# Optimization experiments

Measured on AMD Instinct MI355X. Metric: run time of the kernel, lower is better.

## Reference

```python
import jax, jax.numpy as jnp
import numpy as np

DIM = 1024
NHEAD = 16
HEAD_DIM = DIM // NHEAD
B, S, L = 1, 4096, 4096


def setup_inputs() -> dict:
    key = jax.random.key(0)
    ks = jax.random.split(key, 11)
    scale = 1.0 / np.sqrt(DIM)
    inp = {
        'query': jax.random.normal(ks[0], (B, S, DIM), dtype=jnp.float32),
        'key': jax.random.normal(ks[1], (B, L, DIM), dtype=jnp.float32),
        'value': jax.random.normal(ks[2], (B, L, DIM), dtype=jnp.float32),
        # torch nn.Linear weights: y = x @ W.T + b, W shape (out, in) = (DIM, DIM)
        'Wq': jax.random.normal(ks[3], (DIM, DIM), dtype=jnp.float32) * scale,
        'bq': jax.random.normal(ks[4], (DIM,), dtype=jnp.float32) * 0.01,
        'Wk': jax.random.normal(ks[5], (DIM, DIM), dtype=jnp.float32) * scale,
        'bk': jax.random.normal(ks[6], (DIM,), dtype=jnp.float32) * 0.01,
        'Wv': jax.random.normal(ks[7], (DIM, DIM), dtype=jnp.float32) * scale,
        'bv': jax.random.normal(ks[8], (DIM,), dtype=jnp.float32) * 0.01,
        'Wo': jax.random.normal(ks[9], (DIM, DIM), dtype=jnp.float32) * scale,
        'bo': jax.random.normal(ks[10], (DIM,), dtype=jnp.float32) * 0.01,
    }
    return inp


def _split_heads(x):
    # (B, T, D) -> (B, H, T, hd)
    b, t, _ = x.shape
    return x.reshape(b, t, NHEAD, HEAD_DIM).transpose(0, 2, 1, 3)


def reference(query, key, value, Wq, bq, Wk, bk, Wv, bv, Wo, bo):
    q = _split_heads(query @ Wq.T + bq)   # (B,H,S,hd)
    k = _split_heads(key @ Wk.T + bk)     # (B,H,L,hd)
    v = _split_heads(value @ Wv.T + bv)   # (B,H,L,hd)
    inv_sqrt_d = 1.0 / np.sqrt(HEAD_DIM).astype(np.float32)
    scores = jnp.einsum('bhsd,bhld->bhsl', q, k) * inv_sqrt_d
    probs = jax.nn.softmax(scores, axis=-1)
    ctx = jnp.einsum('bhsl,bhld->bhsd', probs, v)
    ctx = ctx.transpose(0, 2, 1, 3).reshape(query.shape[0], -1, DIM)
    return ctx @ Wo.T + bo
```

## Files before the change

kernel.cpp:

```cpp
#include <hip/hip_runtime.h>
#include <hip/hip_bf16.h>

#define DIM 1024
#define NHEAD 16
#define HD 64
#define SEQ 4096

typedef unsigned short u16;
typedef unsigned int u32;
typedef __attribute__((ext_vector_type(8))) short bf16x8;
typedef __attribute__((ext_vector_type(4))) float f32x4;
typedef __attribute__((ext_vector_type(16))) float f32x16;

__device__ __forceinline__ u16 f2bf(float x) {
  __hip_bfloat16 h = __float2bfloat16(x);
  return *reinterpret_cast<u16*>(&h);
}

__device__ __forceinline__ float bf2f(u16 u) {
  union { u32 u; float f; } c;
  c.u = ((u32)u) << 16;
  return c.f;
}

__device__ __forceinline__ float fexp2(float x) {
#if __has_builtin(__builtin_amdgcn_exp2f)
  return __builtin_amdgcn_exp2f(x);
#else
  return __expf(x * 0.69314718056f);
#endif
}

__device__ __forceinline__ u32 cvtpk(float a, float b) {
  u32 r;
  asm("v_cvt_pk_bf16_f32 %0, %1, %2" : "=v"(r) : "v"(a), "v"(b));
  return r;
}

__device__ __forceinline__ void pswap(u32& a, u32& b) {
  asm("v_permlane32_swap_b32 %0, %1" : "+v"(a), "+v"(b));
}

__device__ __forceinline__ void gload16(const u16* g, const u16* l) {
  __builtin_amdgcn_global_load_lds(
      (const __attribute__((address_space(1))) void*)g,
      (__attribute__((address_space(3))) void*)l, 16, 0, 0);
}

__device__ __forceinline__ float vsum16(const f32x16& v) {
  float a[8];
#pragma unroll
  for (int j = 0; j < 8; ++j) a[j] = v[j] + v[j + 8];
#pragma unroll
  for (int j = 0; j < 4; ++j) a[j] = a[j] + a[j + 4];
  return (a[0] + a[2]) + (a[1] + a[3]);
}

__global__ __launch_bounds__(256) void cvt_all(
    const float* __restrict__ q, const float* __restrict__ k, const float* __restrict__ v,
    const float* __restrict__ wq, const float* __restrict__ wk, const float* __restrict__ wv,
    const float* __restrict__ wo,
    u16* __restrict__ oq, u16* __restrict__ ok, u16* __restrict__ ov,
    u16* __restrict__ owq, u16* __restrict__ owk, u16* __restrict__ owv, u16* __restrict__ owo) {
  int b = blockIdx.x;
  const float* in;
  u16* out;
  int i;
  if (b < 12288) {
    int s = b >> 12;
    in = (s == 0) ? q : (s == 1) ? k : v;
    out = (s == 0) ? oq : (s == 1) ? ok : ov;
    i = (b & 4095) * 256 + threadIdx.x;
  } else {
    int bb = b - 12288;
    int s = bb >> 10;
    in = (s == 0) ? wq : (s == 1) ? wk : (s == 2) ? wv : wo;
    out = (s == 0) ? owq : (s == 1) ? owk : (s == 2) ? owv : owo;
    i = (bb & 1023) * 256 + threadIdx.x;
  }
  float4 val = ((const float4*)in)[i];
  ushort4 o;
  o.x = f2bf(val.x); o.y = f2bf(val.y); o.z = f2bf(val.z); o.w = f2bf(val.w);
  ((ushort4*)out)[i] = o;
}

__global__ __launch_bounds__(256, 3) void gemm_proj(
    const u16* __restrict__ qx, const u16* __restrict__ kx, const u16* __restrict__ vx,
    const u16* __restrict__ wqp, const u16* __restrict__ wkp, const u16* __restrict__ wvp,
    const float* __restrict__ bq, const float* __restrict__ bk, const float* __restrict__ bv,
    u16* __restrict__ Qb, u16* __restrict__ Kb, u16* __restrict__ Vt) {
  __shared__ u16 As[128][64];
  __shared__ u16 Bs[128][64];
  const int z = blockIdx.y;
  const u16 *Ag, *Bg;
  const float* bias;
  u16* outp;
  int mb, nb;
  float scale = 1.f;
  if (z == 0) {
    Ag = qx; Bg = wqp; bias = bq; outp = Qb;
    mb = blockIdx.x >> 3; nb = blockIdx.x & 7; scale = 0.18033688f;
  } else if (z == 1) {
    Ag = kx; Bg = wkp; bias = bk; outp = Kb;
    mb = blockIdx.x >> 3; nb = blockIdx.x & 7;
  } else {
    Ag = wvp; Bg = vx; bias = bv; outp = Vt;
    mb = blockIdx.x >> 5; nb = blockIdx.x & 31;
  }

  const int tid = threadIdx.x, lane = tid & 63, wid = tid >> 6;
  const int lq = lane & 15, g = lane >> 4;
  const int wr = wid >> 1, wc = wid & 1;
  const int m0 = mb * 128, n0 = nb * 128;
  const int sr = lane >> 3, ss = lane & 7;

  const u16* pA = Ag + (size_t)(m0 + wid * 32 + sr) * DIM + ((ss ^ sr) * 8);
  const u16* pB = Bg + (size_t)(n0 + wid * 32 + sr) * DIM + ((ss ^ sr) * 8);

  const f32x4 zero4 = {0.f, 0.f, 0.f, 0.f};
  f32x4 acc[4][4];
#pragma unroll
  for (int mi = 0; mi < 4; ++mi)
#pragma unroll
    for (int ni = 0; ni < 4; ++ni) acc[mi][ni] = zero4;

  for (int k0 = 0; k0 < DIM; k0 += 64) {
    __syncthreads();
#pragma unroll
    for (int i = 0; i < 4; ++i) {
      gload16(pA + i * 8 * DIM + k0, &As[wid * 32 + i * 8][0]);
      gload16(pB + i * 8 * DIM + k0, &Bs[wid * 32 + i * 8][0]);
    }
    __syncthreads();
#pragma unroll
    for (int kk = 0; kk < 2; ++kk) {
      bf16x8 a[4], b[4];
#pragma unroll
      for (int t4 = 0; t4 < 4; ++t4) {
        u32 offA = (u32)(wr * 64 + t4 * 16 + lq) * 128 + (u32)(((kk * 4 + g) ^ (lq & 7)) * 16);
        u32 offB = (u32)(wc * 64 + t4 * 16 + lq) * 128 + (u32)(((kk * 4 + g) ^ (lq & 7)) * 16);
        a[t4] = *(const bf16x8*)((const char*)As + offA);
        b[t4] = *(const bf16x8*)((const char*)Bs + offB);
      }
#pragma unroll
      for (int mi = 0; mi < 4; ++mi)
#pragma unroll
        for (int ni = 0; ni < 4; ++ni)
          acc[mi][ni] = __builtin_amdgcn_mfma_f32_16x16x32_bf16(a[mi], b[ni], acc[mi][ni], 0, 0, 0);
    }
  }

  if (z < 2) {
    float bn[4];
#pragma unroll
    for (int ni = 0; ni < 4; ++ni) bn[ni] = bias[n0 + wc * 64 + ni * 16 + lq];
#pragma unroll
    for (int mi = 0; mi < 4; ++mi)
#pragma unroll
      for (int r = 0; r < 4; ++r) {
        int mm = m0 + wr * 64 + mi * 16 + g * 4 + r;
#pragma unroll
        for (int ni = 0; ni < 4; ++ni) {
          int nn = n0 + wc * 64 + ni * 16 + lq;
          float v = (acc[mi][ni][r] + bn[ni]) * scale;
          outp[((size_t)(nn >> 6) * SEQ + mm) * 64 + (nn & 63)] = f2bf(v);
        }
      }
  } else {
#pragma unroll
    for (int mi = 0; mi < 4; ++mi)
#pragma unroll
      for (int r = 0; r < 4; ++r) {
        int mm = m0 + wr * 64 + mi * 16 + g * 4 + r;
        float bm = bias[mm];
#pragma unroll
        for (int ni = 0; ni < 4; ++ni) {
          int nn = n0 + wc * 64 + ni * 16 + lq;
          outp[(size_t)mm * SEQ + nn] = f2bf(acc[mi][ni][r] + bm);
        }
      }
  }
}

__global__ __launch_bounds__(256) void gemm_out(
    const u16* __restrict__ Ag, const u16* __restrict__ Bg,
    const float* __restrict__ bias, float* __restrict__ outp) {
  __shared__ u16 As[128][64];
  __shared__ u16 Bs[128][64];
  const int tid = threadIdx.x, lane = tid & 63, wid = tid >> 6;
  const int lq = lane & 15, g = lane >> 4;
  const int wr = wid >> 1, wc = wid & 1;
  const int m0 = blockIdx.x * 128, n0 = blockIdx.y * 128;
  const int sr = lane >> 3, ss = lane & 7;

  const u16* pA = Ag + (size_t)(m0 + wid * 32 + sr) * DIM + ((ss ^ sr) * 8);
  const u16* pB = Bg + (size_t)(n0 + wid * 32 + sr) * DIM + ((ss ^ sr) * 8);

  const f32x4 zero4 = {0.f, 0.f, 0.f, 0.f};
  f32x4 acc[4][4];
#pragma unroll
  for (int mi = 0; mi < 4; ++mi)
#pragma unroll
    for (int ni = 0; ni < 4; ++ni) acc[mi][ni] = zero4;

  for (int k0 = 0; k0 < DIM; k0 += 64) {
    __syncthreads();
#pragma unroll
    for (int i = 0; i < 4; ++i) {
      gload16(pA + i * 8 * DIM + k0, &As[wid * 32 + i * 8][0]);
      gload16(pB + i * 8 * DIM + k0, &Bs[wid * 32 + i * 8][0]);
    }
    __syncthreads();
#pragma unroll
    for (int kk = 0; kk < 2; ++kk) {
      bf16x8 a[4], b[4];
#pragma unroll
      for (int t4 = 0; t4 < 4; ++t4) {
        u32 offA = (u32)(wr * 64 + t4 * 16 + lq) * 128 + (u32)(((kk * 4 + g) ^ (lq & 7)) * 16);
        u32 offB = (u32)(wc * 64 + t4 * 16 + lq) * 128 + (u32)(((kk * 4 + g) ^ (lq & 7)) * 16);
        a[t4] = *(const bf16x8*)((const char*)As + offA);
        b[t4] = *(const bf16x8*)((const char*)Bs + offB);
      }
#pragma unroll
      for (int mi = 0; mi < 4; ++mi)
#pragma unroll
        for (int ni = 0; ni < 4; ++ni)
          acc[mi][ni] = __builtin_amdgcn_mfma_f32_16x16x32_bf16(a[mi], b[ni], acc[mi][ni], 0, 0, 0);
    }
  }

  float bn[4];
#pragma unroll
  for (int ni = 0; ni < 4; ++ni) bn[ni] = bias[n0 + wc * 64 + ni * 16 + lq];
#pragma unroll
  for (int mi = 0; mi < 4; ++mi)
#pragma unroll
    for (int r = 0; r < 4; ++r) {
      int mm = m0 + wr * 64 + mi * 16 + g * 4 + r;
#pragma unroll
      for (int ni = 0; ni < 4; ++ni) {
        int nn = n0 + wc * 64 + ni * 16 + lq;
        outp[(size_t)mm * DIM + nn] = acc[mi][ni][r] + bn[ni];
      }
    }
}

__global__ __launch_bounds__(256, 2) void attn32(
    const u16* __restrict__ Qb, const u16* __restrict__ Kb,
    const u16* __restrict__ Vtb, u16* __restrict__ po,
    float* __restrict__ pl) {
  __shared__ u16 Ks[2][64][64];
  __shared__ u16 Vs[2][64][64];
  const int tid = threadIdx.x, lane = tid & 63, wid = tid >> 6;
  const int q5 = lane & 31, hi = lane >> 5;
  const int bid = blockIdx.x;
  const int rest = bid >> 3;
  const int h = (bid & 7) * 2 + (rest >> 5);
  const int kv = (rest >> 4) & 1;
  const int qbase = (rest & 15) * 256 + wid * 64;

  const u16* Qg = Qb + (size_t)h * SEQ * HD;
  const u16* Kg = Kb + (size_t)h * SEQ * HD;
  const u16* Vg = Vtb + (size_t)h * HD * SEQ;

  const int sr = lane >> 3, ss = lane & 7;
  const u16* pK = Kg + (size_t)(kv * 2048 + wid * 16 + sr) * HD + ((ss ^ sr) * 8);
  const u16* pV = Vg + (size_t)(wid * 16 + sr) * SEQ + kv * 2048 + ((ss ^ sr) * 8);

  u32 roff[8];
#pragma unroll
  for (int ks = 0; ks < 4; ++ks) {
    u32 slot = (u32)((ks * 2 + hi) ^ (q5 & 7));
    roff[ks * 2] = (u32)q5 * 128 + slot * 16;
    roff[ks * 2 + 1] = (u32)(32 + q5) * 128 + slot * 16;
  }
  const char* KsB = (const char*)Ks;
  const char* VsB = (const char*)Vs;

  bf16x8 qfA[4], qfB[4];
#pragma unroll
  for (int ks = 0; ks < 4; ++ks) {
    qfA[ks] = *(const bf16x8*)(Qg + (size_t)(qbase + q5) * HD + ks * 16 + hi * 8);
    qfB[ks] = *(const bf16x8*)(Qg + (size_t)(qbase + 32 + q5) * HD + ks * 16 + hi * 8);
  }

  f32x16 oA0, oA1, oB0, oB1, zv;
#pragma unroll
  for (int j = 0; j < 16; ++j) {
    oA0[j] = 0.f; oA1[j] = 0.f; oB0[j] = 0.f; oB1[j] = 0.f; zv[j] = 0.f;
  }
  float lsumA = 0.f, lsumB = 0.f;

  gload16(pK, &Ks[0][wid * 16][0]);
  gload16(pK + 8 * HD, &Ks[0][wid * 16 + 8][0]);
  gload16(pV, &Vs[0][wid * 16][0]);
  gload16(pV + 8 * SEQ, &Vs[0][wid * 16 + 8][0]);
  const u16* pKn = pK + 64 * HD;
  const u16* pVn = pV + 64;
  __syncthreads();

  const int NT = 2048 / 64;

#define PACK_W(W, pk0, pk1)                                                   \
  _Pragma("unroll")                                                           \
  for (int kss = 0; kss < 2; ++kss) {                                         \
    {                                                                         \
      u32 a = pk0[4 * kss], b = pk0[4 * kss + 2];                             \
      u32 c = pk0[4 * kss + 1], d = pk0[4 * kss + 3];                         \
      pswap(a, b);                                                            \
      pswap(c, d);                                                            \
      union { u32 u[4]; bf16x8 v; } tt;                                       \
      tt.u[0] = a; tt.u[1] = c; tt.u[2] = b; tt.u[3] = d;                     \
      W[kss] = tt.v;                                                          \
    }                                                                         \
    {                                                                         \
      u32 a = pk1[4 * kss], b = pk1[4 * kss + 2];                             \
      u32 c = pk1[4 * kss + 1], d = pk1[4 * kss + 3];                         \
      pswap(a, b);                                                            \
      pswap(c, d);                                                            \
      union { u32 u[4]; bf16x8 v; } tt;                                       \
      tt.u[0] = a; tt.u[1] = c; tt.u[2] = b; tt.u[3] = d;                     \
      W[2 + kss] = tt.v;                                                      \
    }                                                                         \
  }

#define ATTN_BODY(CB, PF)                                                       \
  {                                                                             \
    if (PF) {                                                                   \
      gload16(pKn, &Ks[(CB) ^ 1][wid * 16][0]);                                 \
      gload16(pKn + 8 * HD, &Ks[(CB) ^ 1][wid * 16 + 8][0]);                    \
      gload16(pVn, &Vs[(CB) ^ 1][wid * 16][0]);                                 \
      gload16(pVn + 8 * SEQ, &Vs[(CB) ^ 1][wid * 16 + 8][0]);                   \
      pKn += 64 * HD;                                                           \
      pVn += 64;                                                                \
    }                                                                           \
    f32x16 sA0, sA1, sB0, sB1;                                                  \
    __builtin_amdgcn_s_setprio(1);                                              \
    {                                                                           \
      bf16x8 ka0 = *(const bf16x8*)(KsB + (CB) * 8192 + roff[0]);               \
      bf16x8 ka1 = *(const bf16x8*)(KsB + (CB) * 8192 + roff[1]);               \
      sA0 = __builtin_amdgcn_mfma_f32_32x32x16_bf16(ka0, qfA[0], zv, 0, 0, 0);  \
      sA1 = __builtin_amdgcn_mfma_f32_32x32x16_bf16(ka1, qfA[0], zv, 0, 0, 0);  \
      sB0 = __builtin_amdgcn_mfma_f32_32x32x16_bf16(ka0, qfB[0], zv, 0, 0, 0);  \
      sB1 = __builtin_amdgcn_mfma_f32_32x32x16_bf16(ka1, qfB[0], zv, 0, 0, 0);  \
    }                                                                           \
    _Pragma("unroll")                                                           \
    for (int ks = 1; ks < 4; ++ks) {                                            \
      bf16x8 ka0 = *(const bf16x8*)(KsB + (CB) * 8192 + roff[ks * 2]);          \
      bf16x8 ka1 = *(const bf16x8*)(KsB + (CB) * 8192 + roff[ks * 2 + 1]);      \
      sA0 = __builtin_amdgcn_mfma_f32_32x32x16_bf16(ka0, qfA[ks], sA0, 0, 0, 0);\
      sA1 = __builtin_amdgcn_mfma_f32_32x32x16_bf16(ka1, qfA[ks], sA1, 0, 0, 0);\
      sB0 = __builtin_amdgcn_mfma_f32_32x32x16_bf16(ka0, qfB[ks], sB0, 0, 0, 0);\
      sB1 = __builtin_amdgcn_mfma_f32_32x32x16_bf16(ka1, qfB[ks], sB1, 0, 0, 0);\
    }                                                                           \
    __builtin_amdgcn_s_setprio(0);                                              \
    _Pragma("unroll")                                                           \
    for (int j = 0; j < 16; ++j) sA0[j] = fexp2(sA0[j]);                        \
    _Pragma("unroll")                                                           \
    for (int j = 0; j < 16; ++j) sA1[j] = fexp2(sA1[j]);                        \
    _Pragma("unroll")                                                           \
    for (int j = 0; j < 16; ++j) sB0[j] = fexp2(sB0[j]);                        \
    _Pragma("unroll")                                                           \
    for (int j = 0; j < 16; ++j) sB1[j] = fexp2(sB1[j]);                        \
    lsumA += vsum16(sA0) + vsum16(sA1);                                         \
    lsumB += vsum16(sB0) + vsum16(sB1);                                         \
    u32 pkA0[8], pkA1[8], pkB0[8], pkB1[8];                                     \
    _Pragma("unroll")                                                           \
    for (int i2 = 0; i2 < 8; ++i2) {                                            \
      pkA0[i2] = cvtpk(sA0[2 * i2], sA0[2 * i2 + 1]);                           \
      pkA1[i2] = cvtpk(sA1[2 * i2], sA1[2 * i2 + 1]);                           \
      pkB0[i2] = cvtpk(sB0[2 * i2], sB0[2 * i2 + 1]);                           \
      pkB1[i2] = cvtpk(sB1[2 * i2], sB1[2 * i2 + 1]);                           \
    }                                                                           \
    bf16x8 WA[4], WB[4];                                                        \
    PACK_W(WA, pkA0, pkA1)                                                      \
    PACK_W(WB, pkB0, pkB1)                                                      \
    __builtin_amdgcn_s_setprio(1);                                              \
    _Pragma("unroll")                                                           \
    for (int ks = 0; ks < 4; ++ks) {                                            \
      bf16x8 va0 = *(const bf16x8*)(VsB + (CB) * 8192 + roff[ks * 2]);          \
      bf16x8 va1 = *(const bf16x8*)(VsB + (CB) * 8192 + roff[ks * 2 + 1]);      \
      oA0 = __builtin_amdgcn_mfma_f32_32x32x16_bf16(va0, WA[ks], oA0, 0, 0, 0); \
      oA1 = __builtin_amdgcn_mfma_f32_32x32x16_bf16(va1, WA[ks], oA1, 0, 0, 0); \
      oB0 = __builtin_amdgcn_mfma_f32_32x32x16_bf16(va0, WB[ks], oB0, 0, 0, 0); \
      oB1 = __builtin_amdgcn_mfma_f32_32x32x16_bf16(va1, WB[ks], oB1, 0, 0, 0); \
    }                                                                           \
    __builtin_amdgcn_s_setprio(0);                                              \
    __syncthreads();                                                            \
  }

  for (int t = 0; t < NT; t += 2) {
    ATTN_BODY(0, true);
    ATTN_BODY(1, (t + 2 < NT));
  }
#undef ATTN_BODY
#undef PACK_W

  lsumA += __shfl_xor(lsumA, 32);
  lsumB += __shfl_xor(lsumB, 32);
  float invA = 1.f / lsumA;
  float invB = 1.f / lsumB;
  size_t ridxA = (size_t)(kv * 16 + h) * 4096 + qbase + q5;
  size_t ridxB = ridxA + 32;
  u16* cpA = po + ridxA * 64;
  u16* cpB = po + ridxB * 64;
#pragma unroll
  for (int rg = 0; rg < 4; ++rg) {
    ushort4 pa, pb;
    pa.x = f2bf(oA0[rg * 4 + 0] * invA); pa.y = f2bf(oA0[rg * 4 + 1] * invA);
    pa.z = f2bf(oA0[rg * 4 + 2] * invA); pa.w = f2bf(oA0[rg * 4 + 3] * invA);
    pb.x = f2bf(oA1[rg * 4 + 0] * invA); pb.y = f2bf(oA1[rg * 4 + 1] * invA);
    pb.z = f2bf(oA1[rg * 4 + 2] * invA); pb.w = f2bf(oA1[rg * 4 + 3] * invA);
    *(ushort4*)(cpA + rg * 8 + 4 * hi) = pa;
    *(ushort4*)(cpA + 32 + rg * 8 + 4 * hi) = pb;
    pa.x = f2bf(oB0[rg * 4 + 0] * invB); pa.y = f2bf(oB0[rg * 4 + 1] * invB);
    pa.z = f2bf(oB0[rg * 4 + 2] * invB); pa.w = f2bf(oB0[rg * 4 + 3] * invB);
    pb.x = f2bf(oB1[rg * 4 + 0] * invB); pb.y = f2bf(oB1[rg * 4 + 1] * invB);
    pb.z = f2bf(oB1[rg * 4 + 2] * invB); pb.w = f2bf(oB1[rg * 4 + 3] * invB);
    *(ushort4*)(cpB + rg * 8 + 4 * hi) = pa;
    *(ushort4*)(cpB + 32 + rg * 8 + 4 * hi) = pb;
  }
  if (hi == 0) {
    pl[ridxA] = lsumA;
    pl[ridxB] = lsumB;
  }
}

__global__ __launch_bounds__(256) void combine(
    const u16* __restrict__ po, const float* __restrict__ pl,
    u16* __restrict__ cx) {
  const int tid = threadIdx.x;
  const int R = blockIdx.x * 64 + (tid >> 2);
  const int h = R >> 12, q = R & 4095;
  const int dbase = (tid & 3) * 16;
  const int idx0 = R;
  const int idx1 = R + 16 * 4096;
  float l0 = pl[idx0], l1 = pl[idx1];
  float inv = 1.f / (l0 + l1);
  float a0 = l0 * inv, a1 = l1 * inv;
  const u16* p0 = po + (size_t)idx0 * 64 + dbase;
  const u16* p1 = po + (size_t)idx1 * 64 + dbase;
  u16* cp = cx + (size_t)q * DIM + h * 64 + dbase;
#pragma unroll
  for (int v = 0; v < 2; ++v) {
    bf16x8 x0 = *(const bf16x8*)(p0 + v * 8);
    bf16x8 x1 = *(const bf16x8*)(p1 + v * 8);
    union { u16 u[8]; bf16x8 v8; } r;
#pragma unroll
    for (int j = 0; j < 8; ++j)
      r.u[j] = f2bf(a0 * bf2f((u16)x0[j]) + a1 * bf2f((u16)x1[j]));
    *(bf16x8*)(cp + v * 8) = r.v8;
  }
}

extern "C" void kernel_launch(void* const* d_in, const int* in_sizes, int n_in,
                              void* d_out, int out_size, void* d_ws, size_t ws_size,
                              hipStream_t stream) {
  const float* query = (const float*)d_in[0];
  const float* key_  = (const float*)d_in[1];
  const float* value = (const float*)d_in[2];
  const float* Wq = (const float*)d_in[3]; const float* bq = (const float*)d_in[4];
  const float* Wk = (const float*)d_in[5]; const float* bk = (const float*)d_in[6];
  const float* Wv = (const float*)d_in[7]; const float* bv = (const float*)d_in[8];
  const float* Wo = (const float*)d_in[9]; const float* bo = (const float*)d_in[10];

  char* ws = (char*)d_ws;
  const size_t MB = 1024 * 1024;
  u16* qx = (u16*)(ws);
  u16* kx = (u16*)(ws + 8 * MB);
  u16* vx = (u16*)(ws + 16 * MB);
  u16* wq = (u16*)(ws + 24 * MB);
  u16* wk = (u16*)(ws + 26 * MB);
  u16* wv = (u16*)(ws + 28 * MB);
  u16* wo = (u16*)(ws + 30 * MB);
  u16* Qb = (u16*)(ws + 32 * MB);
  u16* Kb = (u16*)(ws + 40 * MB);
  u16* Vt = (u16*)(ws + 48 * MB);
  u16* cx = (u16*)(ws + 56 * MB);
  u16* po = (u16*)(ws);
  float* pl = (float*)(ws + 16 * MB);

  cvt_all<<<dim3(16384), 256, 0, stream>>>(query, key_, value, Wq, Wk, Wv, Wo,
                                           qx, kx, vx, wq, wk, wv, wo);

  gemm_proj<<<dim3(256, 3), 256, 0, stream>>>(qx, kx, vx, wq, wk, wv,
                                              bq, bk, bv, Qb, Kb, Vt);

  attn32<<<dim3(512), 256, 0, stream>>>(Qb, Kb, Vt, po, pl);

  combine<<<dim3(1024), 256, 0, stream>>>(po, pl, cx);

  gemm_out<<<dim3(32, 8), 256, 0, stream>>>(cx, wo, bo, (float*)d_out);
}
```

Before: 156.4 us.

## Software-pipeline attention QK/PV across tiles and shrink output GEMM M-tile

The attention loop is restructured so the QK^T MFMAs for tile t run alongside the PV MFMAs for tile t-1, with a 4-deep K/V shared-memory ring and alternating even/odd P register buffers. The goal is to hide the exp/pack latency between the two matmuls within one iteration. Separately, the output projection GEMM moves to a 64x128 tile with launch bounds of 2 and twice as many blocks, to improve occupancy and wave count on the many CUs. The cost is doubled LDS for K/V in attention (32KB), which may reduce occupancy, plus more register pressure from the extra P buffers.

```diff
diff --git a/kernel.cpp b/kernel.cpp
--- a/kernel.cpp
+++ b/kernel.cpp
@@ -182,47 +182,51 @@
   }
 }
 
-__global__ __launch_bounds__(256) void gemm_out(
+__global__ __launch_bounds__(256, 2) void gemm_out(
     const u16* __restrict__ Ag, const u16* __restrict__ Bg,
     const float* __restrict__ bias, float* __restrict__ outp) {
-  __shared__ u16 As[128][64];
+  __shared__ u16 As[64][64];
   __shared__ u16 Bs[128][64];
   const int tid = threadIdx.x, lane = tid & 63, wid = tid >> 6;
   const int lq = lane & 15, g = lane >> 4;
   const int wr = wid >> 1, wc = wid & 1;
-  const int m0 = blockIdx.x * 128, n0 = blockIdx.y * 128;
+  const int m0 = blockIdx.x * 64, n0 = blockIdx.y * 128;
   const int sr = lane >> 3, ss = lane & 7;
 
-  const u16* pA = Ag + (size_t)(m0 + wid * 32 + sr) * DIM + ((ss ^ sr) * 8);
+  const u16* pA = Ag + (size_t)(m0 + wid * 16 + sr) * DIM + ((ss ^ sr) * 8);
   const u16* pB = Bg + (size_t)(n0 + wid * 32 + sr) * DIM + ((ss ^ sr) * 8);
 
   const f32x4 zero4 = {0.f, 0.f, 0.f, 0.f};
-  f32x4 acc[4][4];
-#pragma unroll
-  for (int mi = 0; mi < 4; ++mi)
+  f32x4 acc[2][4];
+#pragma unroll
+  for (int mi = 0; mi < 2; ++mi)
 #pragma unroll
     for (int ni = 0; ni < 4; ++ni) acc[mi][ni] = zero4;
 
   for (int k0 = 0; k0 < DIM; k0 += 64) {
     __syncthreads();
 #pragma unroll
-    for (int i = 0; i < 4; ++i) {
-      gload16(pA + i * 8 * DIM + k0, &As[wid * 32 + i * 8][0]);
+    for (int i = 0; i < 2; ++i)
+      gload16(pA + i * 8 * DIM + k0, &As[wid * 16 + i * 8][0]);
+#pragma unroll
+    for (int i = 0; i < 4; ++i)
       gload16(pB + i * 8 * DIM + k0, &Bs[wid * 32 + i * 8][0]);
-    }
     __syncthreads();
 #pragma unroll
     for (int kk = 0; kk < 2; ++kk) {
-      bf16x8 a[4], b[4];
+      bf16x8 a[2], b[4];
+#pragma unroll
+      for (int t4 = 0; t4 < 2; ++t4) {
+        u32 offA = (u32)(wr * 32 + t4 * 16 + lq) * 128 + (u32)(((kk * 4 + g) ^ (lq & 7)) * 16);
+        a[t4] = *(const bf16x8*)((const char*)As + offA);
+      }
 #pragma unroll
       for (int t4 = 0; t4 < 4; ++t4) {
-        u32 offA = (u32)(wr * 64 + t4 * 16 + lq) * 128 + (u32)(((kk * 4 + g) ^ (lq & 7)) * 16);
         u32 offB = (u32)(wc * 64 + t4 * 16 + lq) * 128 + (u32)(((kk * 4 + g) ^ (lq & 7)) * 16);
-        a[t4] = *(const bf16x8*)((const char*)As + offA);
         b[t4] = *(const bf16x8*)((const char*)Bs + offB);
       }
 #pragma unroll
-      for (int mi = 0; mi < 4; ++mi)
+      for (int mi = 0; mi < 2; ++mi)
 #pragma unroll
         for (int ni = 0; ni < 4; ++ni)
           acc[mi][ni] = __builtin_amdgcn_mfma_f32_16x16x32_bf16(a[mi], b[ni], acc[mi][ni], 0, 0, 0);
@@ -233,10 +237,10 @@
 #pragma unroll
   for (int ni = 0; ni < 4; ++ni) bn[ni] = bias[n0 + wc * 64 + ni * 16 + lq];
 #pragma unroll
-  for (int mi = 0; mi < 4; ++mi)
+  for (int mi = 0; mi < 2; ++mi)
 #pragma unroll
     for (int r = 0; r < 4; ++r) {
-      int mm = m0 + wr * 64 + mi * 16 + g * 4 + r;
+      int mm = m0 + wr * 32 + mi * 16 + g * 4 + r;
 #pragma unroll
       for (int ni = 0; ni < 4; ++ni) {
         int nn = n0 + wc * 64 + ni * 16 + lq;
@@ -249,8 +253,8 @@
     const u16* __restrict__ Qb, const u16* __restrict__ Kb,
     const u16* __restrict__ Vtb, u16* __restrict__ po,
     float* __restrict__ pl) {
-  __shared__ u16 Ks[2][64][64];
-  __shared__ u16 Vs[2][64][64];
+  __shared__ u16 Ks[4][64][64];
+  __shared__ u16 Vs[4][64][64];
   const int tid = threadIdx.x, lane = tid & 63, wid = tid >> 6;
   const int q5 = lane & 31, hi = lane >> 5;
   const int bid = blockIdx.x;
@@ -290,18 +294,60 @@
     oA0[j] = 0.f; oA1[j] = 0.f; oB0[j] = 0.f; oB1[j] = 0.f; zv[j] = 0.f;
   }
   float lsumA = 0.f, lsumB = 0.f;
-
-  gload16(pK, &Ks[0][wid * 16][0]);
-  gload16(pK + 8 * HD, &Ks[0][wid * 16 + 8][0]);
-  gload16(pV, &Vs[0][wid * 16][0]);
-  gload16(pV + 8 * SEQ, &Vs[0][wid * 16 + 8][0]);
-  const u16* pKn = pK + 64 * HD;
-  const u16* pVn = pV + 64;
-  __syncthreads();
+  f32x16 sA0, sA1, sB0, sB1;
+  bf16x8 WeA[4], WeB[4], WoA[4], WoB[4];
 
   const int NT = 2048 / 64;
 
-#define PACK_W(W, pk0, pk1)                                                   \
+#define PF(tt, cb)                                                            \
+  {                                                                           \
+    const u16* gk = pK + (size_t)(tt) * (64 * HD);                            \
+    const u16* gv = pV + (tt) * 64;                                           \
+    gload16(gk, &Ks[cb][wid * 16][0]);                                        \
+    gload16(gk + 8 * HD, &Ks[cb][wid * 16 + 8][0]);                           \
+    gload16(gv, &Vs[cb][wid * 16][0]);                                        \
+    gload16(gv + 8 * SEQ, &Vs[cb][wid * 16 + 8][0]);                          \
+  }
+
+#define QKSTEP(cb)                                                            \
+  {                                                                           \
+    __builtin_amdgcn_s_setprio(1);                                            \
+    {                                                                         \
+      bf16x8 ka0 = *(const bf16x8*)(KsB + (cb) * 8192 + roff[0]);             \
+      bf16x8 ka1 = *(const bf16x8*)(KsB + (cb) * 8192 + roff[1]);             \
+      sA0 = __builtin_amdgcn_mfma_f32_32x32x16_bf16(ka0, qfA[0], zv, 0, 0, 0);\
+      sA1 = __builtin_amdgcn_mfma_f32_32x32x16_bf16(ka1, qfA[0], zv, 0, 0, 0);\
+      sB0 = __builtin_amdgcn_mfma_f32_32x32x16_bf16(ka0, qfB[0], zv, 0, 0, 0);\
+      sB1 = __builtin_amdgcn_mfma_f32_32x32x16_bf16(ka1, qfB[0], zv, 0, 0, 0);\
+    }                                                                         \
+    _Pragma("unroll")                                                         \
+    for (int ks = 1; ks < 4; ++ks) {                                          \
+      bf16x8 ka0 = *(const bf16x8*)(KsB + (cb) * 8192 + roff[ks * 2]);        \
+      bf16x8 ka1 = *(const bf16x8*)(KsB + (cb) * 8192 + roff[ks * 2 + 1]);    \
+      sA0 = __builtin_amdgcn_mfma_f32_32x32x16_bf16(ka0, qfA[ks], sA0, 0, 0, 0);\
+      sA1 = __builtin_amdgcn_mfma_f32_32x32x16_bf16(ka1, qfA[ks], sA1, 0, 0, 0);\
+      sB0 = __builtin_amdgcn_mfma_f32_32x32x16_bf16(ka0, qfB[ks], sB0, 0, 0, 0);\
+      sB1 = __builtin_amdgcn_mfma_f32_32x32x16_bf16(ka1, qfB[ks], sB1, 0, 0, 0);\
+    }                                                                         \
+    __builtin_amdgcn_s_setprio(0);                                            \
+  }
+
+#define PVSTEP(cb, WA, WB)                                                    \
+  {                                                                           \
+    __builtin_amdgcn_s_setprio(1);                                            \
+    _Pragma("unroll")                                                         \
+    for (int ks = 0; ks < 4; ++ks) {                                          \
+      bf16x8 va0 = *(const bf16x8*)(VsB + (cb) * 8192 + roff[ks * 2]);        \
+      bf16x8 va1 = *(const bf16x8*)(VsB + (cb) * 8192 + roff[ks * 2 + 1]);    \
+      oA0 = __builtin_amdgcn_mfma_f32_32x32x16_bf16(va0, WA[ks], oA0, 0, 0, 0);\
+      oA1 = __builtin_amdgcn_mfma_f32_32x32x16_bf16(va1, WA[ks], oA1, 0, 0, 0);\
+      oB0 = __builtin_amdgcn_mfma_f32_32x32x16_bf16(va0, WB[ks], oB0, 0, 0, 0);\
+      oB1 = __builtin_amdgcn_mfma_f32_32x32x16_bf16(va1, WB[ks], oB1, 0, 0, 0);\
+    }                                                                         \
+    __builtin_amdgcn_s_setprio(0);                                            \
+  }
+
+#define PACK1(W, pk0, pk1)                                                    \
   _Pragma("unroll")                                                           \
   for (int kss = 0; kss < 2; ++kss) {                                         \
     {                                                                         \
@@ -324,77 +370,56 @@
     }                                                                         \
   }
 
-#define ATTN_BODY(CB, PF)                                                       \
-  {                                                                             \
-    if (PF) {                                                                   \
-      gload16(pKn, &Ks[(CB) ^ 1][wid * 16][0]);                                 \
-      gload16(pKn + 8 * HD, &Ks[(CB) ^ 1][wid * 16 + 8][0]);                    \
-      gload16(pVn, &Vs[(CB) ^ 1][wid * 16][0]);                                 \
-      gload16(pVn + 8 * SEQ, &Vs[(CB) ^ 1][wid * 16 + 8][0]);                   \
-      pKn += 64 * HD;                                                           \
-      pVn += 64;                                                                \
-    }                                                                           \
-    f32x16 sA0, sA1, sB0, sB1;                                                  \
-    __builtin_amdgcn_s_setprio(1);                                              \
-    {                                                                           \
-      bf16x8 ka0 = *(const bf16x8*)(KsB + (CB) * 8192 + roff[0]);               \
-      bf16x8 ka1 = *(const bf16x8*)(KsB + (CB) * 8192 + roff[1]);               \
-      sA0 = __builtin_amdgcn_mfma_f32_32x32x16_bf16(ka0, qfA[0], zv, 0, 0, 0);  \
-      sA1 = __builtin_amdgcn_mfma_f32_32x32x16_bf16(ka1, qfA[0], zv, 0, 0, 0);  \
-      sB0 = __builtin_amdgcn_mfma_f32_32x32x16_bf16(ka0, qfB[0], zv, 0, 0, 0);  \
-      sB1 = __builtin_amdgcn_mfma_f32_32x32x16_bf16(ka1, qfB[0], zv, 0, 0, 0);  \
-    }                                                                           \
-    _Pragma("unroll")                                                           \
-    for (int ks = 1; ks < 4; ++ks) {                                            \
-      bf16x8 ka0 = *(const bf16x8*)(KsB + (CB) * 8192 + roff[ks * 2]);          \
-      bf16x8 ka1 = *(const bf16x8*)(KsB + (CB) * 8192 + roff[ks * 2 + 1]);      \
-      sA0 = __builtin_amdgcn_mfma_f32_32x32x16_bf16(ka0, qfA[ks], sA0, 0, 0, 0);\
-      sA1 = __builtin_amdgcn_mfma_f32_32x32x16_bf16(ka1, qfA[ks], sA1, 0, 0, 0);\
-      sB0 = __builtin_amdgcn_mfma_f32_32x32x16_bf16(ka0, qfB[ks], sB0, 0, 0, 0);\
-      sB1 = __builtin_amdgcn_mfma_f32_32x32x16_bf16(ka1, qfB[ks], sB1, 0, 0, 0);\
-    }                                                                           \
-    __builtin_amdgcn_s_setprio(0);                                              \
-    _Pragma("unroll")                                                           \
-    for (int j = 0; j < 16; ++j) sA0[j] = fexp2(sA0[j]);                        \
-    _Pragma("unroll")                                                           \
-    for (int j = 0; j < 16; ++j) sA1[j] = fexp2(sA1[j]);                        \
-    _Pragma("unroll")                                                           \
-    for (int j = 0; j < 16; ++j) sB0[j] = fexp2(sB0[j]);                        \
-    _Pragma("unroll")                                                           \
-    for (int j = 0; j < 16; ++j) sB1[j] = fexp2(sB1[j]);                        \
-    lsumA += vsum16(sA0) + vsum16(sA1);                                         \
-    lsumB += vsum16(sB0) + vsum16(sB1);                                         \
-    u32 pkA0[8], pkA1[8], pkB0[8], pkB1[8];                                     \
-    _Pragma("unroll")                                                           \
-    for (int i2 = 0; i2 < 8; ++i2) {                                            \
-      pkA0[i2] = cvtpk(sA0[2 * i2], sA0[2 * i2 + 1]);                           \
-      pkA1[i2] = cvtpk(sA1[2 * i2], sA1[2 * i2 + 1]);                           \
-      pkB0[i2] = cvtpk(sB0[2 * i2], sB0[2 * i2 + 1]);                           \
-      pkB1[i2] = cvtpk(sB1[2 * i2], sB1[2 * i2 + 1]);                           \
-    }                                                                           \
-    bf16x8 WA[4], WB[4];                                                        \
-    PACK_W(WA, pkA0, pkA1)                                                      \
-    PACK_W(WB, pkB0, pkB1)                                                      \
-    __builtin_amdgcn_s_setprio(1);                                              \
-    _Pragma("unroll")                                                           \
-    for (int ks = 0; ks < 4; ++ks) {                                            \
-      bf16x8 va0 = *(const bf16x8*)(VsB + (CB) * 8192 + roff[ks * 2]);          \
-      bf16x8 va1 = *(const bf16x8*)(VsB + (CB) * 8192 + roff[ks * 2 + 1]);      \
-      oA0 = __builtin_amdgcn_mfma_f32_32x32x16_bf16(va0, WA[ks], oA0, 0, 0, 0); \
-      oA1 = __builtin_amdgcn_mfma_f32_32x32x16_bf16(va1, WA[ks], oA1, 0, 0, 0); \
-      oB0 = __builtin_amdgcn_mfma_f32_32x32x16_bf16(va0, WB[ks], oB0, 0, 0, 0); \
-      oB1 = __builtin_amdgcn_mfma_f32_32x32x16_bf16(va1, WB[ks], oB1, 0, 0, 0); \
-    }                                                                           \
-    __builtin_amdgcn_s_setprio(0);                                              \
-    __syncthreads();                                                            \
-  }
-
-  for (int t = 0; t < NT; t += 2) {
-    ATTN_BODY(0, true);
-    ATTN_BODY(1, (t + 2 < NT));
-  }
-#undef ATTN_BODY
-#undef PACK_W
+#define EXPPACK(WA, WB)                                                       \
+  {                                                                           \
+    _Pragma("unroll")                                                         \
+    for (int j = 0; j < 16; ++j) sA0[j] = fexp2(sA0[j]);                      \
+    _Pragma("unroll")                                                         \
+    for (int j = 0; j < 16; ++j) sA1[j] = fexp2(sA1[j]);                      \
+    _Pragma("unroll")                                                         \
+    for (int j = 0; j < 16; ++j) sB0[j] = fexp2(sB0[j]);                      \
+    _Pragma("unroll")                                                         \
+    for (int j = 0; j < 16; ++j) sB1[j] = fexp2(sB1[j]);                      \
+    lsumA += vsum16(sA0) + vsum16(sA1);                                       \
+    lsumB += vsum16(sB0) + vsum16(sB1);                                       \
+    u32 pkA0[8], pkA1[8], pkB0[8], pkB1[8];                                   \
+    _Pragma("unroll")                                                         \
+    for (int i2 = 0; i2 < 8; ++i2) {                                          \
+      pkA0[i2] = cvtpk(sA0[2 * i2], sA0[2 * i2 + 1]);                         \
+      pkA1[i2] = cvtpk(sA1[2 * i2], sA1[2 * i2 + 1]);                         \
+      pkB0[i2] = cvtpk(sB0[2 * i2], sB0[2 * i2 + 1]);                         \
+      pkB1[i2] = cvtpk(sB1[2 * i2], sB1[2 * i2 + 1]);                         \
+    }                                                                         \
+    PACK1(WA, pkA0, pkA1)                                                     \
+    PACK1(WB, pkB0, pkB1)                                                     \
+  }
+
+#define BODY(r, DO_PF, DO_PV, WCA, WCB, WPA, WPB)                             \
+  {                                                                           \
+    if (DO_PF) PF(tbase + (r) + 1, ((r) + 1) & 3);                            \
+    QKSTEP((r) & 3);                                                          \
+    if (DO_PV) PVSTEP(((r) + 3) & 3, WPA, WPB);                               \
+    EXPPACK(WCA, WCB);                                                        \
+    __syncthreads();                                                          \
+  }
+
+  PF(0, 0);
+  __syncthreads();
+
+  for (int tbase = 0; tbase < NT; tbase += 4) {
+    BODY(0, true, tbase > 0, WeA, WeB, WoA, WoB);
+    BODY(1, true, true, WoA, WoB, WeA, WeB);
+    BODY(2, true, true, WeA, WeB, WoA, WoB);
+    BODY(3, tbase + 4 < NT, true, WoA, WoB, WeA, WeB);
+  }
+  PVSTEP(3, WoA, WoB);
+
+#undef BODY
+#undef EXPPACK
+#undef PACK1
+#undef PVSTEP
+#undef QKSTEP
+#undef PF
 
   lsumA += __shfl_xor(lsumA, 32);
   lsumB += __shfl_xor(lsumB, 32);
@@ -490,5 +515,5 @@
 
   combine<<<dim3(1024), 256, 0, stream>>>(po, pl, cx);
 
-  gemm_out<<<dim3(32, 8), 256, 0, stream>>>(cx, wo, bo, (float*)d_out);
-}
+  gemm_out<<<dim3(64, 8), 256, 0, stream>>>(cx, wo, bo, (float*)d_out);
+}
```

Result: slower. 329.1 us (+110.5%).
